# Kernel optimization log

Measured on AMD Instinct MI355X. Metric: run time of the kernel, lower is better.

Reference implementation:

```python
import jax, jax.numpy as jnp
import numpy as np

S, T, B, IN, H, O = 64, 32, 512, 66, 1024, 1024  # S == max_length


def _gru_cell(x, h, Wih, Whh, bih, bhh):
    # PyTorch GRU cell: gates ordered (r, z, n)
    gi = x @ Wih.T + bih            # [B, 3H]
    gh = h @ Whh.T + bhh            # [B, 3H]
    ir, iz, inn = jnp.split(gi, 3, axis=1)
    hr, hz, hn = jnp.split(gh, 3, axis=1)
    r = jax.nn.sigmoid(ir + hr)
    z = jax.nn.sigmoid(iz + hz)
    n = jnp.tanh(inn + r * hn)
    return (1.0 - z) * n + z * h


def setup_inputs() -> dict:
    key = jax.random.key(0)
    ks = jax.random.split(key, 20)
    s = 0.02
    return {
        "input_tensor": jax.random.normal(ks[0], (S, B, IN), jnp.float32),
        "target_tensor": jax.random.normal(ks[1], (T, B, H), jnp.float32),
        # encoder GRU
        "enc_Wih": jax.random.normal(ks[2], (3 * H, IN), jnp.float32) * s,
        "enc_Whh": jax.random.normal(ks[3], (3 * H, H), jnp.float32) * s,
        "enc_bih": jax.random.normal(ks[4], (3 * H,), jnp.float32) * s,
        "enc_bhh": jax.random.normal(ks[5], (3 * H,), jnp.float32) * s,
        # attention: Linear(2H -> max_length)
        "attn_W": jax.random.normal(ks[6], (S, 2 * H), jnp.float32) * s,
        "attn_b": jax.random.normal(ks[7], (S,), jnp.float32) * s,
        # attn_combine: Linear(2H -> H)
        "comb_W": jax.random.normal(ks[8], (H, 2 * H), jnp.float32) * s,
        "comb_b": jax.random.normal(ks[9], (H,), jnp.float32) * s,
        # decoder GRU
        "dec_Wih": jax.random.normal(ks[10], (3 * H, H), jnp.float32) * s,
        "dec_Whh": jax.random.normal(ks[11], (3 * H, H), jnp.float32) * s,
        "dec_bih": jax.random.normal(ks[12], (3 * H,), jnp.float32) * s,
        "dec_bhh": jax.random.normal(ks[13], (3 * H,), jnp.float32) * s,
        # output: Linear(H -> O)
        "out_W": jax.random.normal(ks[14], (O, H), jnp.float32) * s,
        "out_b": jax.random.normal(ks[15], (O,), jnp.float32) * s,
    }


def reference(input_tensor, target_tensor, enc_Wih, enc_Whh, enc_bih, enc_bhh,
              attn_W, attn_b, comb_W, comb_b, dec_Wih, dec_Whh, dec_bih,
              dec_bhh, out_W, out_b):
    batch = input_tensor.shape[1]
    h0 = jnp.zeros((batch, enc_Whh.shape[1]), input_tensor.dtype)

    # ---- encoder GRU over time ----
    def enc_step(h, x):
        h2 = _gru_cell(x, h, enc_Wih, enc_Whh, enc_bih, enc_bhh)
        return h2, h2

    enc_h, enc_out = jax.lax.scan(enc_step, h0, input_tensor)  # enc_out: [S, B, H]

    # ---- attention decoder, teacher forcing; loop t = 1..T-1 uses target[t-1] ----
    def dec_step(h, x):
        aw = jax.nn.softmax(jnp.concatenate([x, h], axis=1) @ attn_W.T + attn_b,
                            axis=1)                              # [B, S]
        ctx = jnp.einsum('bl,lbh->bh', aw, enc_out)              # [B, H]
        comb = jax.nn.relu(jnp.concatenate([x, ctx], axis=1) @ comb_W.T + comb_b)
        h2 = _gru_cell(comb, h, dec_Wih, dec_Whh, dec_bih, dec_bhh)
        out = jax.nn.log_softmax(h2 @ out_W.T + out_b, axis=1)   # [B, O]
        return h2, out

    _, outs = jax.lax.scan(dec_step, enc_h, target_tensor[:-1])
    # original overwrites `outputs` every step -> only last step survives
    return outs[-1]
```

## Files before the change

kernel.cpp:

```cpp
#include <hip/hip_runtime.h>
#include <hip/hip_bf16.h>
#include <math.h>

#define S_LEN 64
#define T_LEN 32
#define BATCH 512
#define IN_DIM 66
#define INP 128
#define H_DIM 1024
#define O_DIM 1024
#define H3 3072

typedef __attribute__((ext_vector_type(8))) short short8;
typedef __attribute__((ext_vector_type(4))) float f32x4;
typedef __attribute__((ext_vector_type(4))) unsigned short us4;

__device__ __forceinline__ unsigned short f2b(float f) {
    union { float f; unsigned u; } x; x.f = f;
    unsigned r = x.u + 0x7FFF + ((x.u >> 16) & 1);
    return (unsigned short)(r >> 16);
}
__device__ __forceinline__ float b2f(unsigned short s) {
    union { unsigned u; float f; } x; x.u = ((unsigned)s) << 16;
    return x.f;
}
__device__ __forceinline__ void gll16(const void* g, const void* l) {
    __builtin_amdgcn_global_load_lds(
        (const __attribute__((address_space(1))) unsigned int*)g,
        (__attribute__((address_space(3))) unsigned int*)l, 16, 0, 0);
}

template<int TM, int TN>
__global__ __launch_bounds__(256) void gemm_k(
    const unsigned short* __restrict__ A, int lda,
    const unsigned short* __restrict__ W, int ldw,
    const float* __restrict__ bias,
    const float* __restrict__ addf, const unsigned short* __restrict__ addb,
    int ldadd,
    float* __restrict__ Cf,
    unsigned short* __restrict__ Cb, int ldc,
    int K, int flags)
{
    constexpr int IF = TM / 16;
    constexpr int JF = TN / 64;
    constexpr int NW = TN / 4;
    constexpr int CA = TM * 4;
    constexpr int CW = TN * 4;
    __shared__ __align__(16) unsigned short As[2][TM * 32];
    __shared__ __align__(16) unsigned short Bs[2][TN * 32];

    const int bm = blockIdx.y * TM;
    const int bn = blockIdx.x * TN;
    const int t = threadIdx.x;
    const int lane = t & 63;
    const int wv = t >> 6;
    const int ln = lane & 15;
    const int quad = lane >> 4;

    f32x4 acc[IF][JF];
    #pragma unroll
    for (int i = 0; i < IF; i++)
        #pragma unroll
        for (int j = 0; j < JF; j++) {
            f32x4 z = {0.f, 0.f, 0.f, 0.f};
            acc[i][j] = z;
        }

    auto stage = [&](int buf, int k0) {
        if constexpr (CA >= 256) {
            #pragma unroll
            for (int j = 0; j < CA / 256; j++) {
                int ch = j * 256 + t;
                gll16(A + (size_t)(bm + (ch >> 2)) * lda + k0 + (ch & 3) * 8,
                      (const char*)As[buf] + (j * 4 + wv) * 1024);
            }
        } else {
            if (t < CA)
                gll16(A + (size_t)(bm + (t >> 2)) * lda + k0 + (t & 3) * 8,
                      (const char*)As[buf] + wv * 1024);
        }
        if constexpr (CW >= 256) {
            #pragma unroll
            for (int j = 0; j < CW / 256; j++) {
                int ch = j * 256 + t;
                gll16(W + (size_t)(bn + (ch >> 2)) * ldw + k0 + (ch & 3) * 8,
                      (const char*)Bs[buf] + (j * 4 + wv) * 1024);
            }
        } else {
            if (t < CW)
                gll16(W + (size_t)(bn + (t >> 2)) * ldw + k0 + (t & 3) * 8,
                      (const char*)Bs[buf] + wv * 1024);
        }
    };

    const int nt = K >> 5;
    stage(0, 0);
    __syncthreads();
    for (int i = 0; i < nt; ++i) {
        const int cur = i & 1;
        if (i + 1 < nt) stage(cur ^ 1, (i + 1) << 5);
        short8 af[IF], bf[JF];
        #pragma unroll
        for (int ii = 0; ii < IF; ii++)
            af[ii] = *(const short8*)&As[cur][(ii * 16 + ln) * 32 + quad * 8];
        #pragma unroll
        for (int j = 0; j < JF; j++)
            bf[j] = *(const short8*)&Bs[cur][(wv * NW + j * 16 + ln) * 32 + quad * 8];
        #pragma unroll
        for (int ii = 0; ii < IF; ii++)
            #pragma unroll
            for (int j = 0; j < JF; j++)
                acc[ii][j] = __builtin_amdgcn_mfma_f32_16x16x32_bf16(
                    af[ii], bf[j], acc[ii][j], 0, 0, 0);
        __syncthreads();
    }

    #pragma unroll
    for (int i = 0; i < IF; i++) {
        #pragma unroll
        for (int j = 0; j < JF; j++) {
            #pragma unroll
            for (int r = 0; r < 4; r++) {
                int m = bm + i * 16 + quad * 4 + r;
                int n = bn + wv * NW + j * 16 + ln;
                float v = acc[i][j][r];
                if (flags & 1) v += bias[n];
                if (flags & 2) v += addf[(size_t)m * ldadd + n];
                if (flags & 4) v += b2f(addb[(size_t)m * ldadd + n]);
                if (flags & 8) v = fmaxf(v, 0.f);
                if (flags & 16) Cf[(size_t)m * ldc + n] = v;
                if (flags & 32) Cb[(size_t)m * ldc + n] = f2b(v);
            }
        }
    }
}

__device__ __forceinline__ void gru_stage(
    const unsigned short* __restrict__ A, int lda,
    const unsigned short* __restrict__ W, int ldw, int kb,
    unsigned short* As_g, unsigned short* Ws_g,
    int bm, int bn, int gt)
{
    const int gwv = gt >> 6;
    #pragma unroll
    for (int j = 0; j < 2; j++) {
        int ch = j * 128 + gt;
        int s = ch >> 7, r = (ch >> 2) & 31, c = ch & 3;
        gll16(A + (size_t)(bm + r) * lda + kb + s * 32 + c * 8,
              (const char*)As_g + j * 2048 + gwv * 1024);
    }
    #pragma unroll
    for (int j = 0; j < 6; j++) {
        int ch = j * 128 + gt;
        int g = ch >> 8, ch2 = ch & 255;
        int s = ch2 >> 7, w = (ch2 >> 2) & 31, c = ch2 & 3;
        gll16(W + (size_t)(g * H_DIM + bn + w) * ldw + kb + s * 32 + c * 8,
              (const char*)Ws_g + j * 2048 + gwv * 1024);
    }
}

__device__ __forceinline__ void gru_compute(
    const unsigned short* As_g, const unsigned short* Ws_g,
    int gwv, int ln, int quad,
    f32x4 (&accR)[2], f32x4 (&accZ)[2], f32x4 (&accN)[2])
{
    #pragma unroll
    for (int sub = 0; sub < 2; sub++) {
        short8 a[2], bw[3];
        #pragma unroll
        for (int i = 0; i < 2; i++)
            a[i] = *(const short8*)&As_g[sub * 1024 + (i * 16 + ln) * 32 + quad * 8];
        #pragma unroll
        for (int g = 0; g < 3; g++)
            bw[g] = *(const short8*)&Ws_g[g * 2048 + sub * 1024 + (gwv * 16 + ln) * 32 + quad * 8];
        #pragma unroll
        for (int i = 0; i < 2; i++) {
            accR[i] = __builtin_amdgcn_mfma_f32_16x16x32_bf16(a[i], bw[0], accR[i], 0, 0, 0);
            accZ[i] = __builtin_amdgcn_mfma_f32_16x16x32_bf16(a[i], bw[1], accZ[i], 0, 0, 0);
            accN[i] = __builtin_amdgcn_mfma_f32_16x16x32_bf16(a[i], bw[2], accN[i], 0, 0, 0);
        }
    }
}

__global__ __launch_bounds__(256) void gru_gemm(
    const unsigned short* __restrict__ A0, int lda0,
    const unsigned short* __restrict__ W0, int ldw0, int K0,
    const unsigned short* __restrict__ A1,
    const unsigned short* __restrict__ W1,
    const float* __restrict__ bih, const float* __restrict__ bhh,
    const float* __restrict__ hf_in, float* __restrict__ hf_out,
    unsigned short* __restrict__ hb_out, unsigned short* __restrict__ slot)
{
    __shared__ __align__(16) unsigned short As2[2][2][2048];
    __shared__ __align__(16) unsigned short Ws2[2][2][6144];
    const int bn = blockIdx.x * 32;
    const int bm = blockIdx.y * 32;
    const int t = threadIdx.x;
    const int wg = t >> 7;
    const int gt = t & 127;
    const int lane = t & 63;
    const int gwv = gt >> 6;
    const int ln = lane & 15;
    const int quad = lane >> 4;

    f32x4 accR[2], accZ[2], accN0[2], accN1[2];
    #pragma unroll
    for (int i = 0; i < 2; i++) {
        f32x4 z = {0.f, 0.f, 0.f, 0.f};
        accR[i] = z; accZ[i] = z; accN0[i] = z; accN1[i] = z;
    }

    const int half0 = K0 >> 1;
    const int nt0 = half0 >> 6;
    const int nt = nt0 + 8;

    auto stg = [&](int i, int buf) {
        const unsigned short* A; int lda; const unsigned short* W; int ldw; int kb;
        if (i < nt0) { A = A0; lda = lda0; W = W0; ldw = ldw0; kb = wg * half0 + (i << 6); }
        else         { A = A1; lda = H_DIM; W = W1; ldw = H_DIM; kb = wg * 512 + ((i - nt0) << 6); }
        gru_stage(A, lda, W, ldw, kb, As2[wg][buf], Ws2[wg][buf], bm, bn, gt);
    };

    stg(0, 0);
    __syncthreads();
    for (int i = 0; i < nt; ++i) {
        const int cur = i & 1;
        if (i + 1 < nt) stg(i + 1, cur ^ 1);
        if (i < nt0)
            gru_compute(As2[wg][cur], Ws2[wg][cur], gwv, ln, quad, accR, accZ, accN0);
        else
            gru_compute(As2[wg][cur], Ws2[wg][cur], gwv, ln, quad, accR, accZ, accN1);
        __syncthreads();
    }

    float* red = (float*)Ws2;
    const int rb = (gwv * 64 + lane) * 33;
    if (wg == 1) {
        #pragma unroll
        for (int i = 0; i < 2; i++)
            #pragma unroll
            for (int r = 0; r < 4; r++) {
                red[rb + i * 4 + r]      = accR[i][r];
                red[rb + 8 + i * 4 + r]  = accZ[i][r];
                red[rb + 16 + i * 4 + r] = accN0[i][r];
                red[rb + 24 + i * 4 + r] = accN1[i][r];
            }
    }
    __syncthreads();
    if (wg == 0) {
        #pragma unroll
        for (int i = 0; i < 2; i++)
            #pragma unroll
            for (int r = 0; r < 4; r++) {
                accR[i][r]  += red[rb + i * 4 + r];
                accZ[i][r]  += red[rb + 8 + i * 4 + r];
                accN0[i][r] += red[rb + 16 + i * 4 + r];
                accN1[i][r] += red[rb + 24 + i * 4 + r];
            }
        const int n = bn + gwv * 16 + ln;
        const float br = bih[n] + bhh[n];
        const float bz = bih[H_DIM + n] + bhh[H_DIM + n];
        const float bi_n = bih[2 * H_DIM + n];
        const float bh_n = bhh[2 * H_DIM + n];
        #pragma unroll
        for (int i = 0; i < 2; i++) {
            #pragma unroll
            for (int r = 0; r < 4; r++) {
                const int m = bm + i * 16 + quad * 4 + r;
                const size_t idx = (size_t)m * H_DIM + n;
                float rg = 1.f / (1.f + __expf(-(accR[i][r] + br)));
                float zg = 1.f / (1.f + __expf(-(accZ[i][r] + bz)));
                float av = accN0[i][r] + bi_n + rg * (accN1[i][r] + bh_n);
                float e2 = __expf(-2.f * fabsf(av));
                float th = (1.f - e2) / (1.f + e2);
                th = av < 0.f ? -th : th;
                float o = (1.f - zg) * th + zg * hf_in[idx];
                hf_out[idx] = o;
                unsigned short ob = f2b(o);
                hb_out[idx] = ob;
                if (slot) slot[idx] = ob;
            }
        }
    }
}

__global__ __launch_bounds__(256) void attn_ctx(
    const unsigned short* __restrict__ hb,
    const unsigned short* __restrict__ wAhT,
    const unsigned short* __restrict__ attnx_t,
    const unsigned short* __restrict__ encb,
    unsigned short* __restrict__ ctx)
{
    __shared__ float hf[H_DIM];
    __shared__ float part[4][S_LEN];
    __shared__ float awl[S_LEN];
    const int b = blockIdx.x, t = threadIdx.x;
    {
        us4 u = *(const us4*)(hb + ((size_t)b << 10) + t * 4);
        #pragma unroll
        for (int j = 0; j < 4; j++) hf[t * 4 + j] = b2f(u[j]);
    }
    __syncthreads();
    {
        const int c = t & 63, ks = (t >> 6) * 256;
        float s = 0.f;
        #pragma unroll 8
        for (int k = 0; k < 256; k++)
            s += hf[ks + k] * b2f(wAhT[(size_t)(ks + k) * S_LEN + c]);
        part[t >> 6][c] = s;
    }
    __syncthreads();
    if (t < 64) {
        float v = part[0][t] + part[1][t] + part[2][t] + part[3][t]
                + b2f(attnx_t[b * S_LEN + t]);
        float m = v;
        #pragma unroll
        for (int off = 32; off; off >>= 1) m = fmaxf(m, __shfl_xor(m, off));
        float e = __expf(v - m);
        float ss = e;
        #pragma unroll
        for (int off = 32; off; off >>= 1) ss += __shfl_xor(ss, off);
        awl[t] = e / ss;
    }
    __syncthreads();
    const int hq = t * 4;
    float s0 = 0.f, s1 = 0.f, s2 = 0.f, s3 = 0.f;
    #pragma unroll 4
    for (int l = 0; l < S_LEN; l++) {
        us4 u = *(const us4*)(encb + (((size_t)l * BATCH + b) << 10) + hq);
        float w = awl[l];
        s0 += w * b2f(u[0]); s1 += w * b2f(u[1]);
        s2 += w * b2f(u[2]); s3 += w * b2f(u[3]);
    }
    us4 o; o[0] = f2b(s0); o[1] = f2b(s1); o[2] = f2b(s2); o[3] = f2b(s3);
    *(us4*)(ctx + ((size_t)b << 10) + hq) = o;
}

__global__ __launch_bounds__(256) void cvt_all(
    const float* __restrict__ enc_Whh, const float* __restrict__ dec_Wih,
    const float* __restrict__ dec_Whh, const float* __restrict__ comb_W,
    const float* __restrict__ out_W,   const float* __restrict__ attn_W,
    const float* __restrict__ enc_Wih, const float* __restrict__ input,
    const float* __restrict__ target,
    unsigned short* __restrict__ wWhh, unsigned short* __restrict__ wDih,
    unsigned short* __restrict__ wDhh, unsigned short* __restrict__ wCc,
    unsigned short* __restrict__ wCx,  unsigned short* __restrict__ wO,
    unsigned short* __restrict__ wAx,  unsigned short* __restrict__ wAhT,
    unsigned short* __restrict__ wIhp, unsigned short* __restrict__ xbp,
    unsigned short* __restrict__ targetb)
{
    const unsigned nW = H3 * H_DIM / 4;
    const unsigned nH = H_DIM * H_DIM / 4;
    const unsigned nA = S_LEN * H_DIM / 4;
    const unsigned nI = H3 * INP / 4;
    const unsigned nX = S_LEN * BATCH * INP / 4;
    const unsigned nT = T_LEN * BATCH * H_DIM / 4;
    const unsigned total = 3 * nW + 3 * nH + 2 * nA + nI + nX + nT;

    auto plain4 = [](const float* s, unsigned short* d, unsigned i) {
        f32x4 v = *(const f32x4*)(s + (size_t)i * 4);
        us4 o;
        #pragma unroll
        for (int j = 0; j < 4; j++) o[j] = f2b(v[j]);
        *(us4*)(d + (size_t)i * 4) = o;
    };
    auto strided4 = [](const float* s, int ld, int off, int c4s,
                       unsigned short* d, unsigned i) {
        int r = i / c4s, c4 = i - r * c4s;
        f32x4 v = *(const f32x4*)(s + (size_t)r * ld + off + c4 * 4);
        us4 o;
        #pragma unroll
        for (int j = 0; j < 4; j++) o[j] = f2b(v[j]);
        *(us4*)(d + (size_t)i * 4) = o;
    };
    auto pad4 = [](const float* s, unsigned short* d, unsigned i) {
        int r = i >> 5, c = (i & 31) * 4;
        us4 o;
        #pragma unroll
        for (int j = 0; j < 4; j++) {
            int cc = c + j;
            o[j] = (cc < IN_DIM) ? f2b(s[(size_t)r * IN_DIM + cc]) : (unsigned short)0;
        }
        *(us4*)(d + (size_t)r * INP + c) = o;
    };

    for (unsigned q = blockIdx.x * blockDim.x + threadIdx.x; q < total;
         q += gridDim.x * blockDim.x) {
        unsigned i = q;
        if (i < nW) { plain4(enc_Whh, wWhh, i); continue; }  i -= nW;
        if (i < nW) { plain4(dec_Wih, wDih, i); continue; }  i -= nW;
        if (i < nW) { plain4(dec_Whh, wDhh, i); continue; }  i -= nW;
        if (i < nH) { strided4(comb_W, 2 * H_DIM, H_DIM, H_DIM / 4, wCc, i); continue; }  i -= nH;
        if (i < nH) { strided4(comb_W, 2 * H_DIM, 0, H_DIM / 4, wCx, i); continue; }  i -= nH;
        if (i < nH) { plain4(out_W, wO, i); continue; }  i -= nH;
        if (i < nA) { strided4(attn_W, 2 * H_DIM, 0, H_DIM / 4, wAx, i); continue; }  i -= nA;
        if (i < nA) {
            int idx = i * 4, k = idx >> 6, c = idx & 63;
            us4 o;
            #pragma unroll
            for (int j = 0; j < 4; j++)
                o[j] = f2b(attn_W[(size_t)(c + j) * 2 * H_DIM + H_DIM + k]);
            *(us4*)(wAhT + idx) = o;
            continue;
        }  i -= nA;
        if (i < nI) { pad4(enc_Wih, wIhp, i); continue; }  i -= nI;
        if (i < nX) { pad4(input, xbp, i); continue; }  i -= nX;
        plain4(target, targetb, i);
    }
}

__global__ void log_softmax1024(float* __restrict__ x)
{
    __shared__ float red[256];
    float* xr = x + (size_t)blockIdx.x * O_DIM;
    int t = threadIdx.x;
    float m = -1e30f;
    for (int i = t; i < O_DIM; i += 256) m = fmaxf(m, xr[i]);
    red[t] = m; __syncthreads();
    for (int s2 = 128; s2 > 0; s2 >>= 1) {
        if (t < s2) red[t] = fmaxf(red[t], red[t + s2]);
        __syncthreads();
    }
    m = red[0];
    __syncthreads();
    float s = 0.f;
    for (int i = t; i < O_DIM; i += 256) s += expf(xr[i] - m);
    red[t] = s; __syncthreads();
    for (int s2 = 128; s2 > 0; s2 >>= 1) {
        if (t < s2) red[t] += red[t + s2];
        __syncthreads();
    }
    float lse = m + logf(red[0]);
    __syncthreads();
    for (int i = t; i < O_DIM; i += 256) xr[i] = xr[i] - lse;
}

extern "C" void kernel_launch(void* const* d_in, const int* in_sizes, int n_in,
                              void* d_out, int out_size, void* d_ws, size_t ws_size,
                              hipStream_t stream)
{
    const float* input   = (const float*)d_in[0];
    const float* target  = (const float*)d_in[1];
    const float* enc_Wih = (const float*)d_in[2];
    const float* enc_Whh = (const float*)d_in[3];
    const float* enc_bih = (const float*)d_in[4];
    const float* enc_bhh = (const float*)d_in[5];
    const float* attn_W  = (const float*)d_in[6];
    const float* attn_b  = (const float*)d_in[7];
    const float* comb_W  = (const float*)d_in[8];
    const float* comb_b  = (const float*)d_in[9];
    const float* dec_Wih = (const float*)d_in[10];
    const float* dec_Whh = (const float*)d_in[11];
    const float* dec_bih = (const float*)d_in[12];
    const float* dec_bhh = (const float*)d_in[13];
    const float* out_W   = (const float*)d_in[14];
    const float* out_b   = (const float*)d_in[15];
    float* out = (float*)d_out;

    char* p = (char*)d_ws;
    auto alloc = [&](size_t bytes) {
        char* r = p; p += (bytes + 255) & ~(size_t)255; return r;
    };
    unsigned short* wWhh  = (unsigned short*)alloc((size_t)H3 * H_DIM * 2);
    unsigned short* wDih  = (unsigned short*)alloc((size_t)H3 * H_DIM * 2);
    unsigned short* wDhh  = (unsigned short*)alloc((size_t)H3 * H_DIM * 2);
    unsigned short* wCc   = (unsigned short*)alloc((size_t)H_DIM * H_DIM * 2);
    unsigned short* wCx   = (unsigned short*)alloc((size_t)H_DIM * H_DIM * 2);
    unsigned short* wO    = (unsigned short*)alloc((size_t)O_DIM * H_DIM * 2);
    unsigned short* wAhT  = (unsigned short*)alloc((size_t)H_DIM * S_LEN * 2);
    unsigned short* wAx   = (unsigned short*)alloc((size_t)S_LEN * H_DIM * 2);
    unsigned short* wIhp  = (unsigned short*)alloc((size_t)H3 * INP * 2);
    unsigned short* xbp   = (unsigned short*)alloc((size_t)S_LEN * BATCH * INP * 2);
    unsigned short* encb  = (unsigned short*)alloc((size_t)S_LEN * BATCH * H_DIM * 2);
    unsigned short* combx = (unsigned short*)alloc((size_t)(T_LEN - 1) * BATCH * H_DIM * 2);
    unsigned short* attnx = (unsigned short*)alloc((size_t)(T_LEN - 1) * BATCH * S_LEN * 2);
    float*          h     = (float*)alloc((size_t)BATCH * H_DIM * 4);
    unsigned short* hbA   = (unsigned short*)alloc((size_t)BATCH * H_DIM * 2);
    unsigned short* hbB   = (unsigned short*)alloc((size_t)BATCH * H_DIM * 2);
    unsigned short* ctx   = (unsigned short*)alloc((size_t)BATCH * H_DIM * 2);
    unsigned short* comb  = (unsigned short*)alloc((size_t)BATCH * H_DIM * 2);
    unsigned short* targetb = encb;

    const dim3 blk(256);

    hipMemsetAsync(h,   0, (size_t)BATCH * H_DIM * 4, stream);
    hipMemsetAsync(hbA, 0, (size_t)BATCH * H_DIM * 2, stream);

    cvt_all<<<2048, blk, 0, stream>>>(
        enc_Whh, dec_Wih, dec_Whh, comb_W, out_W, attn_W, enc_Wih, input, target,
        wWhh, wDih, wDhh, wCc, wCx, wO, wAx, wAhT, wIhp, xbp, targetb);

    const int MT = (T_LEN - 1) * BATCH;
    gemm_k<64, 64><<<dim3(1, MT / 64), blk, 0, stream>>>(
        targetb, H_DIM, wAx, H_DIM, attn_b,
        nullptr, nullptr, 0, nullptr, attnx, S_LEN, H_DIM, 1 | 32);
    gemm_k<128, 128><<<dim3(H_DIM / 128, MT / 128), blk, 0, stream>>>(
        targetb, H_DIM, wCx, H_DIM, comb_b,
        nullptr, nullptr, 0, nullptr, combx, H_DIM, H_DIM, 1 | 32);

    const dim3 grid_gru(H_DIM / 32, BATCH / 32);
    unsigned short* hcur = hbA;
    unsigned short* hnxt = hbB;

    for (int s = 0; s < S_LEN; s++) {
        gru_gemm<<<grid_gru, blk, 0, stream>>>(
            xbp + (size_t)s * BATCH * INP, INP, wIhp, INP, INP,
            hcur, wWhh, enc_bih, enc_bhh, h, h, hnxt,
            encb + (size_t)s * BATCH * H_DIM);
        unsigned short* tmp = hcur; hcur = hnxt; hnxt = tmp;
    }

    for (int t = 0; t < T_LEN - 1; t++) {
        attn_ctx<<<BATCH, blk, 0, stream>>>(
            hcur, wAhT, attnx + (size_t)t * BATCH * S_LEN, encb, ctx);
        gemm_k<32, 64><<<dim3(H_DIM / 64, BATCH / 32), blk, 0, stream>>>(
            ctx, H_DIM, wCc, H_DIM, nullptr,
            nullptr, combx + (size_t)t * BATCH * H_DIM, H_DIM,
            nullptr, comb, H_DIM, H_DIM, 4 | 8 | 32);
        gru_gemm<<<grid_gru, blk, 0, stream>>>(
            comb, H_DIM, wDih, H_DIM, H_DIM,
            hcur, wDhh, dec_bih, dec_bhh, h, h, hnxt, nullptr);
        unsigned short* tmp = hcur; hcur = hnxt; hnxt = tmp;
    }

    gemm_k<32, 64><<<dim3(O_DIM / 64, BATCH / 32), blk, 0, stream>>>(
        hcur, H_DIM, wO, H_DIM, out_b,
        nullptr, nullptr, 0, out, nullptr, O_DIM, H_DIM, 1 | 16);
    log_softmax1024<<<BATCH, blk, 0, stream>>>(out);
}
```

Baseline: 3.002 ms.

## Use partial vmcnt waits so next-tile loads overlap MFMA compute in GEMMs

```diff
diff --git a/kernel.cpp b/kernel.cpp
--- a/kernel.cpp
+++ b/kernel.cpp
@@ -29,6 +29,15 @@
         (const __attribute__((address_space(1))) unsigned int*)g,
         (__attribute__((address_space(3))) unsigned int*)l, 16, 0, 0);
 }
+template<int N>
+__device__ __forceinline__ void vmwait() {
+    if constexpr (N == 0) asm volatile("s_waitcnt vmcnt(0)" ::: "memory");
+    else if constexpr (N == 2) asm volatile("s_waitcnt vmcnt(2)" ::: "memory");
+    else if constexpr (N == 4) asm volatile("s_waitcnt vmcnt(4)" ::: "memory");
+    else if constexpr (N == 8) asm volatile("s_waitcnt vmcnt(8)" ::: "memory");
+}
+__device__ __forceinline__ void sbar() { __builtin_amdgcn_s_barrier(); }
+__device__ __forceinline__ void schedbar() { __builtin_amdgcn_sched_barrier(0); }
 
 template<int TM, int TN>
 __global__ __launch_bounds__(256) void gemm_k(
@@ -46,6 +55,8 @@
     constexpr int NW = TN / 4;
     constexpr int CA = TM * 4;
     constexpr int CW = TN * 4;
+    constexpr bool PIPE = (CA >= 256) && (CW >= 256);
+    constexpr int PT = (CA + CW) / 256;
     __shared__ __align__(16) unsigned short As[2][TM * 32];
     __shared__ __align__(16) unsigned short Bs[2][TN * 32];
 
@@ -93,12 +104,7 @@
         }
     };
 
-    const int nt = K >> 5;
-    stage(0, 0);
-    __syncthreads();
-    for (int i = 0; i < nt; ++i) {
-        const int cur = i & 1;
-        if (i + 1 < nt) stage(cur ^ 1, (i + 1) << 5);
+    auto comp = [&](int cur) {
         short8 af[IF], bf[JF];
         #pragma unroll
         for (int ii = 0; ii < IF; ii++)
@@ -112,7 +118,31 @@
             for (int j = 0; j < JF; j++)
                 acc[ii][j] = __builtin_amdgcn_mfma_f32_16x16x32_bf16(
                     af[ii], bf[j], acc[ii][j], 0, 0, 0);
+    };
+
+    const int nt = K >> 5;
+    if constexpr (PIPE) {
+        stage(0, 0);
+        for (int i = 0; i < nt; ++i) {
+            const int cur = i & 1;
+            if (i + 1 < nt) { stage(cur ^ 1, (i + 1) << 5); vmwait<PT>(); }
+            else            { vmwait<0>(); }
+            schedbar();
+            sbar();
+            schedbar();
+            comp(cur);
+            schedbar();
+            sbar();
+        }
+    } else {
+        stage(0, 0);
         __syncthreads();
+        for (int i = 0; i < nt; ++i) {
+            const int cur = i & 1;
+            if (i + 1 < nt) stage(cur ^ 1, (i + 1) << 5);
+            comp(cur);
+            __syncthreads();
+        }
     }
 
     #pragma unroll
@@ -222,15 +252,19 @@
     };
 
     stg(0, 0);
-    __syncthreads();
     for (int i = 0; i < nt; ++i) {
         const int cur = i & 1;
-        if (i + 1 < nt) stg(i + 1, cur ^ 1);
+        if (i + 1 < nt) { stg(i + 1, cur ^ 1); vmwait<8>(); }
+        else            { vmwait<0>(); }
+        schedbar();
+        sbar();
+        schedbar();
         if (i < nt0)
             gru_compute(As2[wg][cur], Ws2[wg][cur], gwv, ln, quad, accR, accZ, accN0);
         else
             gru_compute(As2[wg][cur], Ws2[wg][cur], gwv, ln, quad, accR, accZ, accN1);
-        __syncthreads();
+        schedbar();
+        sbar();
     }
 
     float* red = (float*)Ws2;
```

Result: no change. 2.997 ms (-0.2%).
